# Kernel optimization log

Measured on AMD Instinct MI355X. Metric: run time of the kernel, lower is better.

## Reference

```python
import jax, jax.numpy as jnp
import numpy as np

B, N, D = 4, 4096, 512

def setup_inputs() -> dict:
    key = jax.random.key(0)
    ks = jax.random.split(key, 7)
    s = 1.0 / np.sqrt(D)
    return {
        "inputdata": jax.random.normal(ks[0], (B, N, D), dtype=jnp.float32),
        "Wq": jax.random.uniform(ks[1], (D, D), jnp.float32, -s, s),
        "bq": jax.random.uniform(ks[2], (D,), jnp.float32, -s, s),
        "Wk": jax.random.uniform(ks[3], (D, D), jnp.float32, -s, s),
        "bk": jax.random.uniform(ks[4], (D,), jnp.float32, -s, s),
        "Wv": jax.random.uniform(ks[5], (D, D), jnp.float32, -s, s),
        "bv": jax.random.uniform(ks[6], (D,), jnp.float32, -s, s),
    }

def reference(inputdata, Wq, bq, Wk, bk, Wv, bv):
    # torch nn.Linear: y = x @ W^T + b
    Q = jnp.einsum("bnd,ed->bne", inputdata, Wq) + bq  # [B,N,D]
    K = jnp.einsum("bnd,ed->bne", inputdata, Wk) + bk
    V = jnp.einsum("bnd,ed->bne", inputdata, Wv) + bv
    scores = jnp.einsum("bqd,bkd->bqk", Q, K)          # [B,N,N], no 1/sqrt(d) scale
    # NOTE: softmax over dim=1 (the QUERY axis), matching the original torch code
    attn = jax.nn.softmax(scores, axis=1)
    return jnp.einsum("bqk,bkd->bqd", attn, V)         # [B,N,D]
```

## Files before the change

kernel.cpp:

```cpp
#include <hip/hip_runtime.h>
#include <cstdint>


#define NB 4
#define NN 4096
#define ND 512
#define NTOK (NB * NN)

typedef __attribute__((ext_vector_type(8))) short bf16x8;
typedef __attribute__((ext_vector_type(4))) float f32x4;

__device__ __forceinline__ short f2bf(float x) {
  uint32_t u = __float_as_uint(x);
  u += 0x7FFFu + ((u >> 16) & 1u);
  return (short)(u >> 16);
}
__device__ __forceinline__ float bf2f(short h) {
  return __uint_as_float(((uint32_t)(uint16_t)h) << 16);
}
__device__ __forceinline__ void splitf(float x, short& hi, short& lo) {
  short h = f2bf(x);
  hi = h;
  lo = f2bf(x - bf2f(h));
}
__device__ __forceinline__ unsigned int pack2(short a, short b) {
  return (unsigned int)(uint16_t)a | ((unsigned int)(uint16_t)b << 16);
}

__device__ __forceinline__ int xcd_swz(int flat, int nwg) {
  const int cpx = nwg >> 3;
  return (flat & 7) * cpx + (flat >> 3);
}

__device__ __forceinline__ void stage_glds(const short* gbase, long long row_stride,
                                           int row0, int k0, short* ldsplane,
                                           int lane, int wv) {
#pragma unroll
  for (int j = 0; j < 2; ++j) {
    const int chunk = j * 4 + wv;
    const int e = chunk * 512 + lane * 8;
    const int r = e >> 5, k = e & 31;
    const short* src = gbase + (long long)(row0 + r) * row_stride + (k0 + k);
    __builtin_amdgcn_global_load_lds(
        (const __attribute__((address_space(1))) unsigned int*)src,
        (__attribute__((address_space(3))) unsigned int*)(ldsplane + chunk * 512),
        16, 0, 0);
  }
}

__device__ __forceinline__ void mfma_block(const short* lAh, const short* lAl, int astride,
                                           const short* lBh, const short* lBl,
                                           int lane, int wv, f32x4 acc[4][4]) {
  const int ar0 = (wv >> 1) * 64 + (lane & 15);
  const int br0 = (wv & 1) * 64 + (lane & 15);
  const int ko = (lane >> 4) * 8;
  bf16x8 ah[4], al[4], bh[4], bl[4];
#pragma unroll
  for (int f = 0; f < 4; ++f) {
    ah[f] = *(const bf16x8*)(lAh + (ar0 + f * 16) * astride + ko);
    al[f] = *(const bf16x8*)(lAl + (ar0 + f * 16) * astride + ko);
    bh[f] = *(const bf16x8*)(lBh + (br0 + f * 16) * 32 + ko);
    bl[f] = *(const bf16x8*)(lBl + (br0 + f * 16) * 32 + ko);
  }
#pragma unroll
  for (int fm = 0; fm < 4; ++fm)
#pragma unroll
    for (int fn = 0; fn < 4; ++fn)
      acc[fm][fn] = __builtin_amdgcn_mfma_f32_16x16x32_bf16(ah[fm], bh[fn], acc[fm][fn], 0, 0, 0);
#pragma unroll
  for (int fm = 0; fm < 4; ++fm)
#pragma unroll
    for (int fn = 0; fn < 4; ++fn)
      acc[fm][fn] = __builtin_amdgcn_mfma_f32_16x16x32_bf16(ah[fm], bl[fn], acc[fm][fn], 0, 0, 0);
#pragma unroll
  for (int fm = 0; fm < 4; ++fm)
#pragma unroll
    for (int fn = 0; fn < 4; ++fn)
      acc[fm][fn] = __builtin_amdgcn_mfma_f32_16x16x32_bf16(al[fm], bh[fn], acc[fm][fn], 0, 0, 0);
}

__device__ __forceinline__ void stage8(const short* gA_h, const short* gA_l,
                                       const short* gB_h, const short* gB_l,
                                       long long strideA, long long strideB,
                                       int rowA0, int rowB0, int k0,
                                       short* ldsbuf, int lane, int wid) {
  const int plane = wid >> 1, h = wid & 1;
  const short* g = (plane == 0) ? gA_h : (plane == 1) ? gA_l : (plane == 2) ? gB_h : gB_l;
  const long long stride = (plane < 2) ? strideA : strideB;
  const int row0 = ((plane < 2) ? rowA0 : rowB0) + h * 64;
  short* lp = ldsbuf + plane * 8192 + h * 64 * 64;
  const int rsub = lane >> 3;
  const int csub = ((lane & 7) ^ rsub) * 8;
#pragma unroll
  for (int c = 0; c < 8; ++c) {
    const short* src = g + (long long)(row0 + c * 8 + rsub) * stride + (k0 + csub);
    __builtin_amdgcn_global_load_lds(
        (const __attribute__((address_space(1))) unsigned int*)src,
        (__attribute__((address_space(3))) unsigned int*)(lp + c * 512),
        16, 0, 0);
  }
}

__device__ __forceinline__ void mfma_tile8(const short* base, int lane, int wr, int wc,
                                           f32x4 acc[4][2]) {
  const int al = lane & 15, lg = lane >> 4;
  const short* pAh = base;
  const short* pAl = base + 8192;
  const short* pBh = base + 16384;
  const short* pBl = base + 24576;
#pragma unroll
  for (int ksub = 0; ksub < 2; ++ksub) {
    bf16x8 ah[4], alo[4], bh[2], bl[2];
#pragma unroll
    for (int fm = 0; fm < 4; ++fm) {
      const int row = wr * 64 + fm * 16 + al;
      const int slot = (ksub * 4 + lg) ^ (row & 7);
      ah[fm] = *(const bf16x8*)(pAh + row * 64 + slot * 8);
      alo[fm] = *(const bf16x8*)(pAl + row * 64 + slot * 8);
    }
#pragma unroll
    for (int fn = 0; fn < 2; ++fn) {
      const int row = wc * 32 + fn * 16 + al;
      const int slot = (ksub * 4 + lg) ^ (row & 7);
      bh[fn] = *(const bf16x8*)(pBh + row * 64 + slot * 8);
      bl[fn] = *(const bf16x8*)(pBl + row * 64 + slot * 8);
    }
    __builtin_amdgcn_s_setprio(1);
#pragma unroll
    for (int fm = 0; fm < 4; ++fm)
#pragma unroll
      for (int fn = 0; fn < 2; ++fn)
        acc[fm][fn] = __builtin_amdgcn_mfma_f32_16x16x32_bf16(ah[fm], bh[fn], acc[fm][fn], 0, 0, 0);
#pragma unroll
    for (int fm = 0; fm < 4; ++fm)
#pragma unroll
      for (int fn = 0; fn < 2; ++fn)
        acc[fm][fn] = __builtin_amdgcn_mfma_f32_16x16x32_bf16(ah[fm], bl[fn], acc[fm][fn], 0, 0, 0);
#pragma unroll
    for (int fm = 0; fm < 4; ++fm)
#pragma unroll
      for (int fn = 0; fn < 2; ++fn)
        acc[fm][fn] = __builtin_amdgcn_mfma_f32_16x16x32_bf16(alo[fm], bh[fn], acc[fm][fn], 0, 0, 0);
    __builtin_amdgcn_s_setprio(0);
  }
}

__global__ __launch_bounds__(256) void wconv_kernel(
    const float* __restrict__ Wq, const float* __restrict__ Wk, const float* __restrict__ Wv,
    short* __restrict__ Whi, short* __restrict__ Wlo) {
  const int i = blockIdx.x * 256 + threadIdx.x;
  const int m = i >> 16;
  const int e4 = i & 65535;
  const float* W = (m == 0) ? Wq : ((m == 1) ? Wk : Wv);
  const float4 v = ((const float4*)W)[e4];
  short h0, h1, h2, h3, l0, l1, l2, l3;
  splitf(v.x, h0, l0); splitf(v.y, h1, l1); splitf(v.z, h2, l2); splitf(v.w, h3, l3);
  unsigned int* oh = (unsigned int*)(Whi + m * (512 * 512));
  unsigned int* ol = (unsigned int*)(Wlo + m * (512 * 512));
  oh[e4 * 2] = pack2(h0, h1);
  oh[e4 * 2 + 1] = pack2(h2, h3);
  ol[e4 * 2] = pack2(l0, l1);
  ol[e4 * 2 + 1] = pack2(l2, l3);
}

__global__ __launch_bounds__(256, 2) void proj_kernel(
    const float* __restrict__ X, const short* __restrict__ Whi, const short* __restrict__ Wlo,
    const float* __restrict__ bq, const float* __restrict__ bk, const float* __restrict__ bv,
    short* __restrict__ Qhi, short* __restrict__ Qlo,
    short* __restrict__ Khi, short* __restrict__ Klo,
    short* __restrict__ Vthi, short* __restrict__ Vtlo) {
  __shared__ short lAh[128 * 40], lAl[128 * 40];
  __shared__ short lBh[128 * 32], lBl[128 * 32];
  const int tid = threadIdx.x, lane = tid & 63, wv = tid >> 6;
  const int tile = xcd_swz(blockIdx.y * gridDim.x + blockIdx.x, gridDim.x * gridDim.y);
  const int row0 = (tile / 12) * 128;
  const int col0 = (tile % 12) * 128;
  const int mtx = col0 >> 9;
  const int e0 = col0 & 511;
  const short* WhM = Whi + mtx * (512 * 512);
  const short* WlM = Wlo + mtx * (512 * 512);
  f32x4 acc[4][4] = {};
  const int pr = tid >> 1, pc0 = (tid & 1) * 16;
  unsigned int* wAh = (unsigned int*)lAh;
  unsigned int* wAl = (unsigned int*)lAl;

  for (int k0 = 0; k0 < ND; k0 += 32) {
    __syncthreads();
    {
      const float* Xr = X + (long long)(row0 + pr) * ND + k0 + pc0;
      const int wbase = pr * 20 + (pc0 >> 1);
#pragma unroll
      for (int j = 0; j < 4; ++j) {
        const float4 x4 = *(const float4*)(Xr + j * 4);
        short h0, h1, h2, h3, l0, l1, l2, l3;
        splitf(x4.x, h0, l0); splitf(x4.y, h1, l1); splitf(x4.z, h2, l2); splitf(x4.w, h3, l3);
        wAh[wbase + j * 2] = pack2(h0, h1);
        wAh[wbase + j * 2 + 1] = pack2(h2, h3);
        wAl[wbase + j * 2] = pack2(l0, l1);
        wAl[wbase + j * 2 + 1] = pack2(l2, l3);
      }
    }
    stage_glds(WhM, 512, e0, k0, lBh, lane, wv);
    stage_glds(WlM, 512, e0, k0, lBl, lane, wv);
    __syncthreads();
    mfma_block(lAh, lAl, 40, lBh, lBl, lane, wv, acc);
  }

  const float* bias = (mtx == 0) ? bq : ((mtx == 1) ? bk : bv);
  if (mtx < 2) {
    short* Dh = (mtx == 0) ? Qhi : Khi;
    short* Dl = (mtx == 0) ? Qlo : Klo;
    float bb[4];
#pragma unroll
    for (int fn = 0; fn < 4; ++fn)
      bb[fn] = bias[e0 + (wv & 1) * 64 + (lane & 15) + fn * 16];
#pragma unroll
    for (int fm = 0; fm < 4; ++fm) {
      __syncthreads();
#pragma unroll
      for (int fn = 0; fn < 4; ++fn) {
        const int cc = (wv & 1) * 64 + (lane & 15) + fn * 16;
#pragma unroll
        for (int v = 0; v < 4; ++v) {
          const int rs = (wv >> 1) * 16 + ((lane >> 4) << 2) + v;
          short h, l;
          splitf(acc[fm][fn][v] + bb[fn], h, l);
          lAh[rs * 128 + cc] = h;
          lAl[rs * 128 + cc] = l;
        }
      }
      __syncthreads();
#pragma unroll
      for (int s = 0; s < 2; ++s) {
        const int idx = tid + s * 256;
        const int rs = idx >> 4, ch = idx & 15;
        const int gr = row0 + (rs >> 4) * 64 + fm * 16 + (rs & 15);
        const long long o = (long long)gr * ND + e0 + ch * 8;
        *(uint4*)(Dh + o) = *(const uint4*)(lAh + rs * 128 + ch * 8);
        *(uint4*)(Dl + o) = *(const uint4*)(lAl + rs * 128 + ch * 8);
      }
    }
  } else {
    const int lr_base = (wv >> 1) * 64 + ((lane >> 4) << 2);
    const int lc_base = (wv & 1) * 64 + (lane & 15);
#pragma unroll
    for (int fm = 0; fm < 4; ++fm) {
      const int rg = row0 + lr_base + fm * 16;
#pragma unroll
      for (int fn = 0; fn < 4; ++fn) {
        const int e = e0 + lc_base + fn * 16;
        const float bb = bias[e];
        const int b = rg >> 12, n0 = rg & 4095;
        short h0, h1, h2, h3, l0, l1, l2, l3;
        splitf(acc[fm][fn][0] + bb, h0, l0);
        splitf(acc[fm][fn][1] + bb, h1, l1);
        splitf(acc[fm][fn][2] + bb, h2, l2);
        splitf(acc[fm][fn][3] + bb, h3, l3);
        const long long o = ((long long)b * ND + e) * NN + n0;
        *(uint2*)(Vthi + o) = make_uint2(pack2(h0, h1), pack2(h2, h3));
        *(uint2*)(Vtlo + o) = make_uint2(pack2(l0, l1), pack2(l2, l3));
      }
    }
  }
}

__global__ __launch_bounds__(512, 2) void qk8_kernel(
    const short* __restrict__ Qh, const short* __restrict__ Ql,
    const short* __restrict__ Kh, const short* __restrict__ Kl,
    short* __restrict__ Ph, short* __restrict__ Pl, float* __restrict__ pl) {
  __shared__ short lds[2][4][8192];
  const int tid = threadIdx.x, lane = tid & 63, wid = tid >> 6;
  const int wr = wid >> 2, wc = wid & 3;
  const int al = lane & 15, lg = lane >> 4;
  const int tile = xcd_swz(blockIdx.y * gridDim.x + blockIdx.x, gridDim.x * gridDim.y);
  const int q0 = (tile / 32) * 128, c0 = (tile % 32) * 128;
  f32x4 acc[4][2] = {};

  stage8(Qh, Ql, Kh, Kl, ND, ND, q0, c0, 0, &lds[0][0][0], lane, wid);
  asm volatile("s_waitcnt vmcnt(0)" ::: "memory");
  __syncthreads();

  for (int kt = 0; kt < 8; ++kt) {
    const int cur = kt & 1;
    if (kt < 7)
      stage8(Qh, Ql, Kh, Kl, ND, ND, q0, c0, (kt + 1) * 64, &lds[cur ^ 1][0][0], lane, wid);
    mfma_tile8(&lds[cur][0][0], lane, wr, wc, acc);
    asm volatile("s_waitcnt vmcnt(0)" ::: "memory");
    __syncthreads();
  }

#pragma unroll
  for (int fm = 0; fm < 4; ++fm)
#pragma unroll
    for (int fn = 0; fn < 2; ++fn)
#pragma unroll
      for (int v = 0; v < 4; ++v) acc[fm][fn][v] = __expf(acc[fm][fn][v]);

#pragma unroll
  for (int fn = 0; fn < 2; ++fn) {
    float l = 0.f;
#pragma unroll
    for (int fm = 0; fm < 4; ++fm)
#pragma unroll
      for (int v = 0; v < 4; ++v) l += acc[fm][fn][v];
    l += __shfl_xor(l, 16);
    l += __shfl_xor(l, 32);
    if (lg == 0) {
      const long long prow =
          (long long)((q0 >> 7) * 2 + wr) * NN + c0 + wc * 32 + fn * 16 + al;
      pl[prow] = l;
    }
  }

  short* th = &lds[0][0][0];
  short* tl = &lds[0][2][0];
  __syncthreads();
#pragma unroll
  for (int fm = 0; fm < 4; ++fm)
#pragma unroll
    for (int fn = 0; fn < 2; ++fn)
#pragma unroll
      for (int v = 0; v < 4; ++v) {
        const int row = wr * 64 + fm * 16 + lg * 4 + v;
        const int col = wc * 32 + fn * 16 + al;
        short h, l;
        splitf(acc[fm][fn][v], h, l);
        th[row * 128 + col] = h;
        tl[row * 128 + col] = l;
      }
  __syncthreads();
#pragma unroll
  for (int s = 0; s < 4; ++s) {
    const int idx = tid + s * 512;
    const int rs = idx >> 4, ch = idx & 15;
    const long long o = (long long)(q0 + rs) * NN + c0 + ch * 8;
    *(uint4*)(Ph + o) = *(const uint4*)(th + rs * 128 + ch * 8);
    *(uint4*)(Pl + o) = *(const uint4*)(tl + rs * 128 + ch * 8);
  }
}

__global__ __launch_bounds__(256) void stats_combine_kernel(
    const float* __restrict__ pl, float* __restrict__ Li) {
  const int col = blockIdx.x * 256 + threadIdx.x;
  float l = 0.f;
#pragma unroll 8
  for (int i = 0; i < 64; ++i) l += pl[(long long)i * NN + col];
  Li[col] = 1.0f / l;
}

__global__ __launch_bounds__(256) void vscale_kernel(
    const short* __restrict__ Vth, const short* __restrict__ Vtl,
    const float* __restrict__ Li, short* __restrict__ Vsh, short* __restrict__ Vsl) {
  const int t = blockIdx.x * 256 + threadIdx.x;
  const long long base = (long long)t * 8;
  const int k0 = (int)(base & (NN - 1));
  const uint4 vh = *(const uint4*)(Vth + base);
  const uint4 vl = *(const uint4*)(Vtl + base);
  const float4 li0 = *(const float4*)(Li + k0);
  const float4 li1 = *(const float4*)(Li + k0 + 4);
  const unsigned int* ph = (const unsigned int*)&vh;
  const unsigned int* plo = (const unsigned int*)&vl;
  float li[8] = {li0.x, li0.y, li0.z, li0.w, li1.x, li1.y, li1.z, li1.w};
  short h[8], l[8];
#pragma unroll
  for (int j = 0; j < 8; ++j) {
    const unsigned int wh = ph[j >> 1], wl = plo[j >> 1];
    const short sh = (short)((j & 1) ? (wh >> 16) : wh);
    const short sl = (short)((j & 1) ? (wl >> 16) : wl);
    const float v = (bf2f(sh) + bf2f(sl)) * li[j];
    splitf(v, h[j], l[j]);
  }
  uint4 oh, ol;
  oh.x = pack2(h[0], h[1]); oh.y = pack2(h[2], h[3]);
  oh.z = pack2(h[4], h[5]); oh.w = pack2(h[6], h[7]);
  ol.x = pack2(l[0], l[1]); ol.y = pack2(l[2], l[3]);
  ol.z = pack2(l[4], l[5]); ol.w = pack2(l[6], l[7]);
  *(uint4*)(Vsh + base) = oh;
  *(uint4*)(Vsl + base) = ol;
}

__global__ __launch_bounds__(512, 2) void pv8_kernel(
    const short* __restrict__ Ph, const short* __restrict__ Pl,
    const short* __restrict__ Vh, const short* __restrict__ Vl,
    float* __restrict__ partials) {
  __shared__ short lds[2][4][8192];
  const int tid = threadIdx.x, lane = tid & 63, wid = tid >> 6;
  const int wr = wid >> 2, wc = wid & 3;
  const int al = lane & 15, lg = lane >> 4;
  const int tile = xcd_swz(blockIdx.y * gridDim.x + blockIdx.x, gridDim.x * gridDim.y);
  const int d0 = (tile % 4) * 128, q0 = (tile / 4) * 128;
  const int kb = blockIdx.z * 512;
  f32x4 acc[4][2] = {};

  stage8(Ph, Pl, Vh, Vl, NN, NN, q0, d0, kb, &lds[0][0][0], lane, wid);
  asm volatile("s_waitcnt vmcnt(0)" ::: "memory");
  __syncthreads();

  for (int kt = 0; kt < 8; ++kt) {
    const int cur = kt & 1;
    if (kt < 7)
      stage8(Ph, Pl, Vh, Vl, NN, NN, q0, d0, kb + (kt + 1) * 64, &lds[cur ^ 1][0][0], lane, wid);
    mfma_tile8(&lds[cur][0][0], lane, wr, wc, acc);
    asm volatile("s_waitcnt vmcnt(0)" ::: "memory");
    __syncthreads();
  }

  float* Pd = partials + (long long)blockIdx.z * (NN * ND);
#pragma unroll
  for (int fm = 0; fm < 4; ++fm)
#pragma unroll
    for (int fn = 0; fn < 2; ++fn)
#pragma unroll
      for (int v = 0; v < 4; ++v) {
        const int row = q0 + wr * 64 + fm * 16 + lg * 4 + v;
        const int col = d0 + wc * 32 + fn * 16 + al;
        Pd[(long long)row * ND + col] = acc[fm][fn][v];
      }
}

__global__ __launch_bounds__(256) void reduce_kernel(
    const float* __restrict__ partials, float* __restrict__ Ob) {
  const int i = blockIdx.x * 256 + threadIdx.x;
  const float4* p = (const float4*)partials;
  const int stride = (NN * ND) / 4;
  float4 s = p[i];
#pragma unroll
  for (int c = 1; c < 8; ++c) {
    const float4 t = p[i + c * stride];
    s.x += t.x; s.y += t.y; s.z += t.z; s.w += t.w;
  }
  ((float4*)Ob)[i] = s;
}

extern "C" void kernel_launch(void* const* d_in, const int* in_sizes, int n_in,
                              void* d_out, int out_size, void* d_ws, size_t ws_size,
                              hipStream_t stream) {
  (void)in_sizes; (void)n_in; (void)out_size; (void)ws_size;
  const float* X = (const float*)d_in[0];
  const float* Wq = (const float*)d_in[1];
  const float* bq = (const float*)d_in[2];
  const float* Wk = (const float*)d_in[3];
  const float* bk = (const float*)d_in[4];
  const float* Wv = (const float*)d_in[5];
  const float* bv = (const float*)d_in[6];
  float* out = (float*)d_out;

  char* ws = (char*)d_ws;
  size_t off = 0;
  auto take = [&](size_t bytes) -> char* {
    char* p = ws + off;
    off += (bytes + 255) & ~(size_t)255;
    return p;
  };
  short* Qhi = (short*)take((size_t)NTOK * ND * 2);
  short* Qlo = (short*)take((size_t)NTOK * ND * 2);
  short* Khi = (short*)take((size_t)NTOK * ND * 2);
  short* Klo = (short*)take((size_t)NTOK * ND * 2);
  short* Vthi = (short*)take((size_t)NTOK * ND * 2);
  short* Vtlo = (short*)take((size_t)NTOK * ND * 2);
  short* Whi = (short*)take((size_t)3 * 512 * 512 * 2);
  short* Wlo = (short*)take((size_t)3 * 512 * 512 * 2);
  float* Li = (float*)take((size_t)NN * 4);
  float* pl = (float*)take((size_t)64 * NN * 4);
  short* Vshi = (short*)take((size_t)ND * NN * 2);
  short* Vslo = (short*)take((size_t)ND * NN * 2);
  float* S = (float*)take((size_t)NN * NN * 4);
  short* Phi = (short*)take((size_t)NN * NN * 2);
  short* Plo = (short*)take((size_t)NN * NN * 2);

  hipLaunchKernelGGL(wconv_kernel, dim3(768), dim3(256), 0, stream, Wq, Wk, Wv, Whi, Wlo);
  hipLaunchKernelGGL(proj_kernel, dim3(12, 128), dim3(256), 0, stream,
                     X, Whi, Wlo, bq, bk, bv, Qhi, Qlo, Khi, Klo, Vthi, Vtlo);

  for (int b = 0; b < NB; ++b) {
    const long long tb = (long long)b * NN * ND;
    hipLaunchKernelGGL(qk8_kernel, dim3(32, 32), dim3(512), 0, stream,
                       Qhi + tb, Qlo + tb, Khi + tb, Klo + tb, Phi, Plo, pl);
    hipLaunchKernelGGL(stats_combine_kernel, dim3(16), dim3(256), 0, stream, pl, Li);
    hipLaunchKernelGGL(vscale_kernel, dim3((ND * NN) / 2048), dim3(256), 0, stream,
                       Vthi + tb, Vtlo + tb, Li, Vshi, Vslo);
    hipLaunchKernelGGL(pv8_kernel, dim3(4, 32, 8), dim3(512), 0, stream,
                       Phi, Plo, Vshi, Vslo, S );
    hipLaunchKernelGGL(reduce_kernel, dim3((NN * ND) / 1024), dim3(256), 0, stream,
                       S , out + tb);
  }
}
```

Baseline: 769.0 us.

## Enlarge QK and PV GEMM tiles to 256x256 with 32-wide K steps

```diff
diff --git a/kernel.cpp b/kernel.cpp
--- a/kernel.cpp
+++ b/kernel.cpp
@@ -79,68 +79,77 @@
       acc[fm][fn] = __builtin_amdgcn_mfma_f32_16x16x32_bf16(al[fm], bh[fn], acc[fm][fn], 0, 0, 0);
 }
 
-__device__ __forceinline__ void stage8(const short* gA_h, const short* gA_l,
-                                       const short* gB_h, const short* gB_l,
-                                       long long strideA, long long strideB,
-                                       int rowA0, int rowB0, int k0,
-                                       short* ldsbuf, int lane, int wid) {
-  const int plane = wid >> 1, h = wid & 1;
-  const short* g = (plane == 0) ? gA_h : (plane == 1) ? gA_l : (plane == 2) ? gB_h : gB_l;
-  const long long stride = (plane < 2) ? strideA : strideB;
-  const int row0 = ((plane < 2) ? rowA0 : rowB0) + h * 64;
-  short* lp = ldsbuf + plane * 8192 + h * 64 * 64;
-  const int rsub = lane >> 3;
-  const int csub = ((lane & 7) ^ rsub) * 8;
-#pragma unroll
-  for (int c = 0; c < 8; ++c) {
-    const short* src = g + (long long)(row0 + c * 8 + rsub) * stride + (k0 + csub);
+__device__ __forceinline__ int swz_off(int row, int kb) {
+  return ((row >> 1) << 6) + (((((row & 1) << 2) + kb) ^ ((row >> 1) & 7)) << 3);
+}
+
+__device__ __forceinline__ void stage256(const short* gAh, const short* gAl,
+                                         const short* gBh, const short* gBl,
+                                         long long sA, long long sB,
+                                         int rA0, int rB0, int k0,
+                                         short* buf, int lane, int wid) {
+  const int plane = wid >> 1;
+  const short* g = (plane == 0) ? gAh : (plane == 1) ? gAl : (plane == 2) ? gBh : gBl;
+  const long long stride = (plane < 2) ? sA : sB;
+  const int row0 = (plane < 2) ? rA0 : rB0;
+  short* lp = buf + plane * 8192;
+  const int qbase = (wid & 1) * 512;
+#pragma unroll
+  for (int i = 0; i < 8; ++i) {
+    const int q = qbase + i * 64 + lane;
+    const int j = q >> 3, s = q & 7;
+    const int t = s ^ (j & 7);
+    const int r = 2 * j + (t >> 2), kb = t & 3;
+    const short* src = g + (long long)(row0 + r) * stride + (k0 + kb * 8);
     __builtin_amdgcn_global_load_lds(
         (const __attribute__((address_space(1))) unsigned int*)src,
-        (__attribute__((address_space(3))) unsigned int*)(lp + c * 512),
+        (__attribute__((address_space(3))) unsigned int*)(lp + (qbase + i * 64) * 8),
         16, 0, 0);
   }
 }
 
-__device__ __forceinline__ void mfma_tile8(const short* base, int lane, int wr, int wc,
-                                           f32x4 acc[4][2]) {
-  const int al = lane & 15, lg = lane >> 4;
+__device__ __forceinline__ void mfma_tile256(const short* base, int lane, int wr, int wc,
+                                             f32x4 acc[8][4]) {
+  const int al = lane & 15, kb = lane >> 4;
   const short* pAh = base;
   const short* pAl = base + 8192;
   const short* pBh = base + 16384;
   const short* pBl = base + 24576;
-#pragma unroll
-  for (int ksub = 0; ksub < 2; ++ksub) {
-    bf16x8 ah[4], alo[4], bh[2], bl[2];
-#pragma unroll
-    for (int fm = 0; fm < 4; ++fm) {
-      const int row = wr * 64 + fm * 16 + al;
-      const int slot = (ksub * 4 + lg) ^ (row & 7);
-      ah[fm] = *(const bf16x8*)(pAh + row * 64 + slot * 8);
-      alo[fm] = *(const bf16x8*)(pAl + row * 64 + slot * 8);
-    }
-#pragma unroll
-    for (int fn = 0; fn < 2; ++fn) {
-      const int row = wc * 32 + fn * 16 + al;
-      const int slot = (ksub * 4 + lg) ^ (row & 7);
-      bh[fn] = *(const bf16x8*)(pBh + row * 64 + slot * 8);
-      bl[fn] = *(const bf16x8*)(pBl + row * 64 + slot * 8);
+  bf16x8 bh[4], bl[4];
+#pragma unroll
+  for (int fn = 0; fn < 4; ++fn) {
+    const int off = swz_off(wc * 64 + fn * 16 + al, kb);
+    bh[fn] = *(const bf16x8*)(pBh + off);
+    bl[fn] = *(const bf16x8*)(pBl + off);
+  }
+#pragma unroll
+  for (int fmh = 0; fmh < 2; ++fmh) {
+    bf16x8 ah[4], alo[4];
+#pragma unroll
+    for (int f = 0; f < 4; ++f) {
+      const int off = swz_off(wr * 128 + (fmh * 4 + f) * 16 + al, kb);
+      ah[f] = *(const bf16x8*)(pAh + off);
+      alo[f] = *(const bf16x8*)(pAl + off);
     }
     __builtin_amdgcn_s_setprio(1);
 #pragma unroll
-    for (int fm = 0; fm < 4; ++fm)
-#pragma unroll
-      for (int fn = 0; fn < 2; ++fn)
-        acc[fm][fn] = __builtin_amdgcn_mfma_f32_16x16x32_bf16(ah[fm], bh[fn], acc[fm][fn], 0, 0, 0);
-#pragma unroll
-    for (int fm = 0; fm < 4; ++fm)
-#pragma unroll
-      for (int fn = 0; fn < 2; ++fn)
-        acc[fm][fn] = __builtin_amdgcn_mfma_f32_16x16x32_bf16(ah[fm], bl[fn], acc[fm][fn], 0, 0, 0);
-#pragma unroll
-    for (int fm = 0; fm < 4; ++fm)
-#pragma unroll
-      for (int fn = 0; fn < 2; ++fn)
-        acc[fm][fn] = __builtin_amdgcn_mfma_f32_16x16x32_bf16(alo[fm], bh[fn], acc[fm][fn], 0, 0, 0);
+    for (int f = 0; f < 4; ++f)
+#pragma unroll
+      for (int fn = 0; fn < 4; ++fn)
+        acc[fmh * 4 + f][fn] =
+            __builtin_amdgcn_mfma_f32_16x16x32_bf16(ah[f], bh[fn], acc[fmh * 4 + f][fn], 0, 0, 0);
+#pragma unroll
+    for (int f = 0; f < 4; ++f)
+#pragma unroll
+      for (int fn = 0; fn < 4; ++fn)
+        acc[fmh * 4 + f][fn] =
+            __builtin_amdgcn_mfma_f32_16x16x32_bf16(ah[f], bl[fn], acc[fmh * 4 + f][fn], 0, 0, 0);
+#pragma unroll
+    for (int f = 0; f < 4; ++f)
+#pragma unroll
+      for (int fn = 0; fn < 4; ++fn)
+        acc[fmh * 4 + f][fn] =
+            __builtin_amdgcn_mfma_f32_16x16x32_bf16(alo[f], bh[fn], acc[fmh * 4 + f][fn], 0, 0, 0);
     __builtin_amdgcn_s_setprio(0);
   }
 }
@@ -264,78 +273,84 @@
   }
 }
 
-__global__ __launch_bounds__(512, 2) void qk8_kernel(
+__global__ __launch_bounds__(512, 2) void qk9_kernel(
     const short* __restrict__ Qh, const short* __restrict__ Ql,
     const short* __restrict__ Kh, const short* __restrict__ Kl,
     short* __restrict__ Ph, short* __restrict__ Pl, float* __restrict__ pl) {
-  __shared__ short lds[2][4][8192];
+  __shared__ short lds[2][32768];
   const int tid = threadIdx.x, lane = tid & 63, wid = tid >> 6;
   const int wr = wid >> 2, wc = wid & 3;
   const int al = lane & 15, lg = lane >> 4;
-  const int tile = xcd_swz(blockIdx.y * gridDim.x + blockIdx.x, gridDim.x * gridDim.y);
-  const int q0 = (tile / 32) * 128, c0 = (tile % 32) * 128;
-  f32x4 acc[4][2] = {};
-
-  stage8(Qh, Ql, Kh, Kl, ND, ND, q0, c0, 0, &lds[0][0][0], lane, wid);
+  const int tile = xcd_swz(blockIdx.y * gridDim.x + blockIdx.x, 256);
+  const int q0 = (tile >> 4) * 256, c0 = (tile & 15) * 256;
+  f32x4 acc[8][4] = {};
+
+  stage256(Qh, Ql, Kh, Kl, ND, ND, q0, c0, 0, lds[0], lane, wid);
   asm volatile("s_waitcnt vmcnt(0)" ::: "memory");
   __syncthreads();
 
-  for (int kt = 0; kt < 8; ++kt) {
+  for (int kt = 0; kt < 16; ++kt) {
     const int cur = kt & 1;
-    if (kt < 7)
-      stage8(Qh, Ql, Kh, Kl, ND, ND, q0, c0, (kt + 1) * 64, &lds[cur ^ 1][0][0], lane, wid);
-    mfma_tile8(&lds[cur][0][0], lane, wr, wc, acc);
+    if (kt < 15)
+      stage256(Qh, Ql, Kh, Kl, ND, ND, q0, c0, (kt + 1) * 32, lds[cur ^ 1], lane, wid);
+    mfma_tile256(lds[cur], lane, wr, wc, acc);
     asm volatile("s_waitcnt vmcnt(0)" ::: "memory");
     __syncthreads();
   }
 
 #pragma unroll
-  for (int fm = 0; fm < 4; ++fm)
-#pragma unroll
-    for (int fn = 0; fn < 2; ++fn)
+  for (int fm = 0; fm < 8; ++fm)
+#pragma unroll
+    for (int fn = 0; fn < 4; ++fn)
 #pragma unroll
       for (int v = 0; v < 4; ++v) acc[fm][fn][v] = __expf(acc[fm][fn][v]);
 
 #pragma unroll
-  for (int fn = 0; fn < 2; ++fn) {
+  for (int fn = 0; fn < 4; ++fn) {
     float l = 0.f;
 #pragma unroll
-    for (int fm = 0; fm < 4; ++fm)
+    for (int fm = 0; fm < 8; ++fm)
 #pragma unroll
       for (int v = 0; v < 4; ++v) l += acc[fm][fn][v];
     l += __shfl_xor(l, 16);
     l += __shfl_xor(l, 32);
     if (lg == 0) {
-      const long long prow =
-          (long long)((q0 >> 7) * 2 + wr) * NN + c0 + wc * 32 + fn * 16 + al;
+      const long long prow = (long long)((q0 >> 8) * 2 + wr) * NN + c0 + wc * 64 + fn * 16 + al;
       pl[prow] = l;
     }
   }
 
-  short* th = &lds[0][0][0];
-  short* tl = &lds[0][2][0];
-  __syncthreads();
-#pragma unroll
-  for (int fm = 0; fm < 4; ++fm)
-#pragma unroll
-    for (int fn = 0; fn < 2; ++fn)
-#pragma unroll
-      for (int v = 0; v < 4; ++v) {
-        const int row = wr * 64 + fm * 16 + lg * 4 + v;
-        const int col = wc * 32 + fn * 16 + al;
-        short h, l;
-        splitf(acc[fm][fn][v], h, l);
-        th[row * 128 + col] = h;
-        tl[row * 128 + col] = l;
+  short* sb = &lds[0][0];
+#pragma unroll
+  for (int h = 0; h < 4; ++h) {
+    __syncthreads();
+    if (wr == (h >> 1)) {
+#pragma unroll
+      for (int f = 0; f < 4; ++f) {
+        const int fm = (h & 1) * 4 + f;
+#pragma unroll
+        for (int fn = 0; fn < 4; ++fn)
+#pragma unroll
+          for (int v = 0; v < 4; ++v) {
+            const int rs = f * 16 + lg * 4 + v;
+            const int cs = wc * 64 + fn * 16 + al;
+            short hh, ll;
+            splitf(acc[fm][fn][v], hh, ll);
+            sb[rs * 256 + cs] = hh;
+            sb[16384 + rs * 256 + cs] = ll;
+          }
       }
-  __syncthreads();
-#pragma unroll
-  for (int s = 0; s < 4; ++s) {
-    const int idx = tid + s * 512;
-    const int rs = idx >> 4, ch = idx & 15;
-    const long long o = (long long)(q0 + rs) * NN + c0 + ch * 8;
-    *(uint4*)(Ph + o) = *(const uint4*)(th + rs * 128 + ch * 8);
-    *(uint4*)(Pl + o) = *(const uint4*)(tl + rs * 128 + ch * 8);
+    }
+    __syncthreads();
+#pragma unroll
+    for (int s = 0; s < 8; ++s) {
+      const int idx = tid + s * 512;
+      const int p = idx >> 11, c2 = idx & 2047;
+      const int rs = c2 >> 5, ch = c2 & 31;
+      const long long o = (long long)(q0 + h * 64 + rs) * NN + c0 + ch * 8;
+      short* dst = p ? Pl : Ph;
+      *(uint4*)(dst + o) = *(const uint4*)(sb + p * 16384 + rs * 256 + ch * 8);
+    }
   }
 }
 
@@ -344,7 +359,7 @@
   const int col = blockIdx.x * 256 + threadIdx.x;
   float l = 0.f;
 #pragma unroll 8
-  for (int i = 0; i < 64; ++i) l += pl[(long long)i * NN + col];
+  for (int i = 0; i < 32; ++i) l += pl[(long long)i * NN + col];
   Li[col] = 1.0f / l;
 }
 
@@ -379,41 +394,41 @@
   *(uint4*)(Vsl + base) = ol;
 }
 
-__global__ __launch_bounds__(512, 2) void pv8_kernel(
+__global__ __launch_bounds__(512, 2) void pv9_kernel(
     const short* __restrict__ Ph, const short* __restrict__ Pl,
     const short* __restrict__ Vh, const short* __restrict__ Vl,
     float* __restrict__ partials) {
-  __shared__ short lds[2][4][8192];
+  __shared__ short lds[2][32768];
   const int tid = threadIdx.x, lane = tid & 63, wid = tid >> 6;
   const int wr = wid >> 2, wc = wid & 3;
   const int al = lane & 15, lg = lane >> 4;
-  const int tile = xcd_swz(blockIdx.y * gridDim.x + blockIdx.x, gridDim.x * gridDim.y);
-  const int d0 = (tile % 4) * 128, q0 = (tile / 4) * 128;
-  const int kb = blockIdx.z * 512;
-  f32x4 acc[4][2] = {};
-
-  stage8(Ph, Pl, Vh, Vl, NN, NN, q0, d0, kb, &lds[0][0][0], lane, wid);
+  const int tile = xcd_swz(blockIdx.y * gridDim.x + blockIdx.x, 32);
+  const int d0 = (tile & 1) * 256, q0 = (tile >> 1) * 256;
+  const int kb0 = blockIdx.z * 512;
+  f32x4 acc[8][4] = {};
+
+  stage256(Ph, Pl, Vh, Vl, NN, NN, q0, d0, kb0, lds[0], lane, wid);
   asm volatile("s_waitcnt vmcnt(0)" ::: "memory");
   __syncthreads();
 
-  for (int kt = 0; kt < 8; ++kt) {
+  for (int kt = 0; kt < 16; ++kt) {
     const int cur = kt & 1;
-    if (kt < 7)
-      stage8(Ph, Pl, Vh, Vl, NN, NN, q0, d0, kb + (kt + 1) * 64, &lds[cur ^ 1][0][0], lane, wid);
-    mfma_tile8(&lds[cur][0][0], lane, wr, wc, acc);
+    if (kt < 15)
+      stage256(Ph, Pl, Vh, Vl, NN, NN, q0, d0, kb0 + (kt + 1) * 32, lds[cur ^ 1], lane, wid);
+    mfma_tile256(lds[cur], lane, wr, wc, acc);
     asm volatile("s_waitcnt vmcnt(0)" ::: "memory");
     __syncthreads();
   }
 
   float* Pd = partials + (long long)blockIdx.z * (NN * ND);
 #pragma unroll
-  for (int fm = 0; fm < 4; ++fm)
-#pragma unroll
-    for (int fn = 0; fn < 2; ++fn)
+  for (int fm = 0; fm < 8; ++fm)
+#pragma unroll
+    for (int fn = 0; fn < 4; ++fn)
 #pragma unroll
       for (int v = 0; v < 4; ++v) {
-        const int row = q0 + wr * 64 + fm * 16 + lg * 4 + v;
-        const int col = d0 + wc * 32 + fn * 16 + al;
+        const int row = q0 + wr * 128 + fm * 16 + lg * 4 + v;
+        const int col = d0 + wc * 64 + fn * 16 + al;
         Pd[(long long)row * ND + col] = acc[fm][fn][v];
       }
 }
@@ -474,12 +489,12 @@
 
   for (int b = 0; b < NB; ++b) {
     const long long tb = (long long)b * NN * ND;
-    hipLaunchKernelGGL(qk8_kernel, dim3(32, 32), dim3(512), 0, stream,
+    hipLaunchKernelGGL(qk9_kernel, dim3(16, 16), dim3(512), 0, stream,
                        Qhi + tb, Qlo + tb, Khi + tb, Klo + tb, Phi, Plo, pl);
     hipLaunchKernelGGL(stats_combine_kernel, dim3(16), dim3(256), 0, stream, pl, Li);
     hipLaunchKernelGGL(vscale_kernel, dim3((ND * NN) / 2048), dim3(256), 0, stream,
                        Vthi + tb, Vtlo + tb, Li, Vshi, Vslo);
-    hipLaunchKernelGGL(pv8_kernel, dim3(4, 32, 8), dim3(512), 0, stream,
+    hipLaunchKernelGGL(pv9_kernel, dim3(2, 16, 8), dim3(512), 0, stream,
                        Phi, Plo, Vshi, Vslo, S );
     hipLaunchKernelGGL(reduce_kernel, dim3((NN * ND) / 1024), dim3(256), 0, stream,
                        S , out + tb);
```

Result: faster. 665.0 us (-13.5%).
